# Performance work log

Hardware: AMD Instinct MI355X
Metric: run time of the kernel (lower is better)

## Reference

```python
import jax, jax.numpy as jnp
import numpy as np

N_SPARSE = 2  # keep N of every M weights (2:4 structured sparsity)
M_SPARSE = 4


def compute_mask(w, n, m):
    # w: [out, in]; zero the (m - n) smallest-|w| entries in each group of m
    out_f, in_f = w.shape
    k = m - n
    wr = jnp.abs(w).reshape(out_f, in_f // m, m)
    # indices of the k smallest |w| per group (torch.topk largest=False)
    _, idx = jax.lax.top_k(-wr, k)                      # [out, in/m, k]
    pruned = jax.nn.one_hot(idx, m, dtype=w.dtype).sum(axis=-2)  # [out, in/m, m]
    mask = 1.0 - pruned
    return mask.reshape(out_f, in_f)


def setup_inputs() -> dict:
    key = jax.random.key(0)
    k1, k2, k3 = jax.random.split(key, 3)
    B, S, Din, Dout = 64, 197, 768, 3072
    x = jax.random.normal(k1, (B, S, Din), dtype=jnp.float32)
    weight = jax.random.normal(k2, (Dout, Din), dtype=jnp.float32)
    bias = jax.random.normal(k3, (Dout,), dtype=jnp.float32)
    return {"x": x, "weight": weight, "bias": bias}


def reference(x, weight, bias):
    # mask is a precomputed buffer in torch (not differentiated)
    mask = compute_mask(jax.lax.stop_gradient(weight), N_SPARSE, M_SPARSE)
    w = weight * mask
    # F.linear: x @ w.T + b
    return jnp.einsum('bsi,oi->bso', x, w) + bias
```

## Files before the change

### kernel.cpp

```cpp
#include <hip/hip_runtime.h>
#include <hip/hip_bf16.h>

#define M_DIM 12608
#define K_DIM 768
#define N_DIM 3072
#define M_PAD 12800
#define BM 128
#define BN 128
#define BK 32
#define NT (K_DIM / BK)
#define MBLK (M_PAD / BM)
#define NBLK (N_DIM / BN)
#define NWG (MBLK * NBLK)

typedef __attribute__((ext_vector_type(8))) short bf16x8;
typedef __attribute__((ext_vector_type(4))) float f32x4;

__device__ __forceinline__ void gload_lds16(const void* g, void* l) {
  __builtin_amdgcn_global_load_lds(
      (const __attribute__((address_space(1))) unsigned int*)g,
      (__attribute__((address_space(3))) unsigned int*)l,
      16, 0, 0);
}

#define GX 4800
#define GW 2304
__global__ void cvt_fused(const float* __restrict__ x, const float* __restrict__ w,
                          __hip_bfloat16* __restrict__ xb, __hip_bfloat16* __restrict__ wb) {
  if (blockIdx.x < GX) {
    size_t i = ((size_t)blockIdx.x * 256 + threadIdx.x) * 8;
    union { __hip_bfloat16 h[8]; uint4 u; } o;
    if (i < (size_t)M_DIM * K_DIM) {
      float4 a = *(const float4*)(x + i);
      float4 b = *(const float4*)(x + i + 4);
      o.h[0] = __float2bfloat16(a.x); o.h[1] = __float2bfloat16(a.y);
      o.h[2] = __float2bfloat16(a.z); o.h[3] = __float2bfloat16(a.w);
      o.h[4] = __float2bfloat16(b.x); o.h[5] = __float2bfloat16(b.y);
      o.h[6] = __float2bfloat16(b.z); o.h[7] = __float2bfloat16(b.w);
    } else {
      o.u = make_uint4(0, 0, 0, 0);
    }
    *(uint4*)(xb + i) = o.u;
  } else {
    size_t g = ((size_t)(blockIdx.x - GX) * 256 + threadIdx.x);
    float4 v = *(const float4*)(w + g * 4);
    float val[4] = {v.x, v.y, v.z, v.w};
    float a[4] = {fabsf(v.x), fabsf(v.y), fabsf(v.z), fabsf(v.w)};
    union { __hip_bfloat16 h[4]; uint2 u; } o;
#pragma unroll
    for (int i = 0; i < 4; ++i) {
      int rank = 0;
#pragma unroll
      for (int j = 0; j < 4; ++j)
        rank += (a[j] > a[i]) || (a[j] == a[i] && j > i);
      o.h[i] = __float2bfloat16(rank < 2 ? val[i] : 0.0f);
    }
    *(uint2*)(wb + g * 4) = o.u;
  }
}

__global__ __launch_bounds__(256, 4) void gemm_bt(
    const __hip_bfloat16* __restrict__ A,
    const __hip_bfloat16* __restrict__ B,
    const float* __restrict__ bias,
    float* __restrict__ C)
{
  __shared__ char smem[32768];

  const int tid  = threadIdx.x;
  const int lane = tid & 63;
  const int wave = tid >> 6;
  const int wm   = wave >> 1;
  const int wn   = wave & 1;

  const int wg  = blockIdx.x;
  const int swz = (wg & 7) * (NWG / 8) + (wg >> 3);
  const int tile_m = (swz / NBLK) * BM;
  const int tile_n = (swz % NBLK) * BN;

  const int r2 = lane >> 2;
  const int p  = lane & 3;
  const int gsw = p ^ (r2 & 3) ^ ((r2 >> 2) & 3);
  const __hip_bfloat16* asrc[2];
  const __hip_bfloat16* bsrc[2];
#pragma unroll
  for (int u = 0; u < 2; ++u) {
    const int row = wave * 32 + u * 16 + r2;
    asrc[u] = A + (size_t)(tile_m + row) * K_DIM + gsw * 8;
    bsrc[u] = B + (size_t)(tile_n + row) * K_DIM + gsw * 8;
  }

  const int frow  = lane & 15;
  const int fslot = (lane >> 4) ^ (frow & 3) ^ ((frow >> 2) & 3);
  const int abase = (wm * 64 + frow) * 64 + fslot * 16;
  const int bbase = 8192 + (wn * 64 + frow) * 64 + fslot * 16;

  f32x4 acc[4][4] = {};

#pragma unroll
  for (int u = 0; u < 2; ++u)
    gload_lds16(asrc[u], smem + (wave * 2 + u) * 1024);
#pragma unroll
  for (int u = 0; u < 2; ++u)
    gload_lds16(bsrc[u], smem + 8192 + (wave * 2 + u) * 1024);

  for (int t = 0; t < NT; ++t) {
    __syncthreads();

    if (t + 1 < NT) {
      char* nb = smem + ((t + 1) & 1) * 16384;
      const int off = (t + 1) * BK;
#pragma unroll
      for (int u = 0; u < 2; ++u)
        gload_lds16(asrc[u] + off, nb + (wave * 2 + u) * 1024);
#pragma unroll
      for (int u = 0; u < 2; ++u)
        gload_lds16(bsrc[u] + off, nb + 8192 + (wave * 2 + u) * 1024);
    }

    const char* bq = smem + (t & 1) * 16384;
    bf16x8 af[4], bfv[4];
#pragma unroll
    for (int m = 0; m < 4; ++m)
      af[m] = *(const bf16x8*)(bq + abase + m * 1024);
#pragma unroll
    for (int n = 0; n < 4; ++n)
      bfv[n] = *(const bf16x8*)(bq + bbase + n * 1024);
#pragma unroll
    for (int m = 0; m < 4; ++m)
#pragma unroll
      for (int n = 0; n < 4; ++n)
        acc[m][n] = __builtin_amdgcn_mfma_f32_16x16x32_bf16(af[m], bfv[n], acc[m][n], 0, 0, 0);
  }

  const int ccol = lane & 15;
  const int quad = lane >> 4;
  float bv[4];
#pragma unroll
  for (int n = 0; n < 4; ++n)
    bv[n] = bias[tile_n + wn * 64 + n * 16 + ccol];

#pragma unroll
  for (int m = 0; m < 4; ++m) {
    const int rbase = tile_m + wm * 64 + m * 16 + quad * 4;
#pragma unroll
    for (int r = 0; r < 4; ++r) {
      const int grow = rbase + r;
      if (grow < M_DIM) {
        float* crow = C + (size_t)grow * N_DIM + tile_n + wn * 64;
#pragma unroll
        for (int n = 0; n < 4; ++n)
          crow[n * 16 + ccol] = acc[m][n][r] + bv[n];
      }
    }
  }
}

extern "C" void kernel_launch(void* const* d_in, const int* in_sizes, int n_in,
                              void* d_out, int out_size, void* d_ws, size_t ws_size,
                              hipStream_t stream) {
  const float* x    = (const float*)d_in[0];
  const float* w    = (const float*)d_in[1];
  const float* bias = (const float*)d_in[2];
  float* out = (float*)d_out;

  __hip_bfloat16* xb = (__hip_bfloat16*)d_ws;
  __hip_bfloat16* wb = xb + (size_t)M_PAD * K_DIM;

  cvt_fused<<<GX + GW, 256, 0, stream>>>(x, w, xb, wb);
  gemm_bt<<<NWG, 256, 0, stream>>>(xb, wb, bias, out);
}
```

Baseline: 249.0 us.

## Rewrite GEMM as 256x256 tile, 8-wave ping-pong pipeline with barriers and setprio

Replaces the 128x128 tile, 4-wave GEMM with a 256x256x64 tile run by 8 waves over 128KB of dynamic LDS. The loop interleaves staged global-to-LDS loads with MFMA quarters, using explicit vmcnt waits, barriers and s_setprio to overlap memory traffic with matrix math. The larger tiles raise arithmetic intensity and cut redundant global loads. The cost is more registers per thread (acc[8][4]), lower occupancy, fewer workgroups (50x12=600) which can hurt wave quantization, and fragile hand-written synchronisation.

```diff
diff --git a/kernel.cpp b/kernel.cpp
--- a/kernel.cpp
+++ b/kernel.cpp
@@ -5,9 +5,9 @@
 #define K_DIM 768
 #define N_DIM 3072
 #define M_PAD 12800
-#define BM 128
-#define BN 128
-#define BK 32
+#define BM 256
+#define BN 256
+#define BK 64
 #define NT (K_DIM / BK)
 #define MBLK (M_PAD / BM)
 #define NBLK (N_DIM / BN)
@@ -59,78 +59,117 @@
   }
 }
 
-__global__ __launch_bounds__(256, 4) void gemm_bt(
+__global__ __launch_bounds__(512, 2) void gemm_8p(
     const __hip_bfloat16* __restrict__ A,
     const __hip_bfloat16* __restrict__ B,
     const float* __restrict__ bias,
     float* __restrict__ C)
 {
-  __shared__ char smem[32768];
+  extern __shared__ char smem[];
 
   const int tid  = threadIdx.x;
   const int lane = tid & 63;
   const int wave = tid >> 6;
-  const int wm   = wave >> 1;
-  const int wn   = wave & 1;
+  const int wm   = wave >> 2;
+  const int wn   = wave & 3;
 
   const int wg  = blockIdx.x;
   const int swz = (wg & 7) * (NWG / 8) + (wg >> 3);
-  const int tile_m = (swz / NBLK) * BM;
-  const int tile_n = (swz % NBLK) * BN;
-
-  const int r2 = lane >> 2;
-  const int p  = lane & 3;
-  const int gsw = p ^ (r2 & 3) ^ ((r2 >> 2) & 3);
-  const __hip_bfloat16* asrc[2];
-  const __hip_bfloat16* bsrc[2];
-#pragma unroll
-  for (int u = 0; u < 2; ++u) {
-    const int row = wave * 32 + u * 16 + r2;
-    asrc[u] = A + (size_t)(tile_m + row) * K_DIM + gsw * 8;
-    bsrc[u] = B + (size_t)(tile_n + row) * K_DIM + gsw * 8;
-  }
-
-  const int frow  = lane & 15;
-  const int fslot = (lane >> 4) ^ (frow & 3) ^ ((frow >> 2) & 3);
-  const int abase = (wm * 64 + frow) * 64 + fslot * 16;
-  const int bbase = 8192 + (wn * 64 + frow) * 64 + fslot * 16;
-
-  f32x4 acc[4][4] = {};
-
-#pragma unroll
-  for (int u = 0; u < 2; ++u)
-    gload_lds16(asrc[u], smem + (wave * 2 + u) * 1024);
-#pragma unroll
-  for (int u = 0; u < 2; ++u)
-    gload_lds16(bsrc[u], smem + 8192 + (wave * 2 + u) * 1024);
-
-  for (int t = 0; t < NT; ++t) {
-    __syncthreads();
-
-    if (t + 1 < NT) {
-      char* nb = smem + ((t + 1) & 1) * 16384;
-      const int off = (t + 1) * BK;
-#pragma unroll
-      for (int u = 0; u < 2; ++u)
-        gload_lds16(asrc[u] + off, nb + (wave * 2 + u) * 1024);
-#pragma unroll
-      for (int u = 0; u < 2; ++u)
-        gload_lds16(bsrc[u] + off, nb + 8192 + (wave * 2 + u) * 1024);
-    }
-
-    const char* bq = smem + (t & 1) * 16384;
-    bf16x8 af[4], bfv[4];
-#pragma unroll
-    for (int m = 0; m < 4; ++m)
-      af[m] = *(const bf16x8*)(bq + abase + m * 1024);
-#pragma unroll
-    for (int n = 0; n < 4; ++n)
-      bfv[n] = *(const bf16x8*)(bq + bbase + n * 1024);
-#pragma unroll
-    for (int m = 0; m < 4; ++m)
-#pragma unroll
-      for (int n = 0; n < 4; ++n)
-        acc[m][n] = __builtin_amdgcn_mfma_f32_16x16x32_bf16(af[m], bfv[n], acc[m][n], 0, 0, 0);
+  const int tile_m = (swz % MBLK) * BM;
+  const int tile_n = (swz / MBLK) * BN;
+
+  const int l4 = lane >> 2;
+  const int gk = ((lane & 3) ^ ((lane >> 3) & 3)) * 8;
+  const __hip_bfloat16* ag = A + (size_t)(tile_m + wave * 16 + l4) * K_DIM + gk;
+  const __hip_bfloat16* bg = B + (size_t)(tile_n + wave * 16 + l4) * K_DIM + gk;
+
+#define STG_A(T, kh) { \
+    char* d_ = smem + (((T) & 1) << 16) + ((kh) << 14) + (wave << 10); \
+    gload_lds16(ag + (size_t)(T) * BK + (kh) * 32, d_); \
+    gload_lds16(ag + (size_t)128 * K_DIM + (size_t)(T) * BK + (kh) * 32, d_ + 8192); }
+#define STG_B(T, kh) { \
+    char* d_ = smem + (((T) & 1) << 16) + 32768 + ((kh) << 14) + (wave << 10); \
+    gload_lds16(bg + (size_t)(T) * BK + (kh) * 32, d_); \
+    gload_lds16(bg + (size_t)128 * K_DIM + (size_t)(T) * BK + (kh) * 32, d_ + 8192); }
+#define BAR() { __builtin_amdgcn_s_barrier(); asm volatile("" ::: "memory"); }
+#define VM(n) asm volatile("s_waitcnt vmcnt(" #n ")" ::: "memory")
+
+  const int frow = lane & 15;
+  const int fsl  = (((lane >> 4) ^ ((frow >> 1) & 3)) << 4);
+  const char* aL = smem + (wm * 128 + frow) * 64 + fsl;
+  const char* bL = smem + 32768 + (wn * 64 + frow) * 64 + fsl;
+
+  f32x4 acc[8][4] = {};
+  bf16x8 af[4], bfv[4];
+
+#define MFMA_Q(mbase) \
+    _Pragma("unroll") for (int m = 0; m < 4; ++m) \
+    _Pragma("unroll") for (int n = 0; n < 4; ++n) \
+      acc[(mbase) + m][n] = __builtin_amdgcn_mfma_f32_16x16x32_bf16(af[m], bfv[n], acc[(mbase) + m][n], 0, 0, 0);
+#define LD_A(db, kh, mbase) \
+    _Pragma("unroll") for (int m = 0; m < 4; ++m) \
+      af[m] = *(const bf16x8*)(aL + (db) + ((kh) << 14) + ((mbase) + m) * 1024);
+#define LD_B(db, kh) \
+    _Pragma("unroll") for (int n = 0; n < 4; ++n) \
+      bfv[n] = *(const bf16x8*)(bL + (db) + ((kh) << 14) + n * 1024);
+
+  STG_A(0, 0); STG_B(0, 0); STG_A(0, 1); STG_B(0, 1); STG_A(1, 0); STG_B(1, 0);
+  VM(8);
+  BAR();
+
+#pragma unroll 2
+  for (int t = 0; t < NT - 2; ++t) {
+    const int db = (t & 1) << 16;
+    LD_A(db, 0, 0); LD_B(db, 0);
+    STG_A(t + 1, 1);
+    BAR();
+    __builtin_amdgcn_s_setprio(1); MFMA_Q(0); __builtin_amdgcn_s_setprio(0);
+    BAR();
+    LD_A(db, 0, 4);
+    STG_B(t + 1, 1);
+    BAR();
+    __builtin_amdgcn_s_setprio(1); MFMA_Q(4); __builtin_amdgcn_s_setprio(0);
+    VM(8);
+    BAR();
+    LD_A(db, 1, 0); LD_B(db, 1);
+    STG_A(t + 2, 0);
+    BAR();
+    __builtin_amdgcn_s_setprio(1); MFMA_Q(0); __builtin_amdgcn_s_setprio(0);
+    BAR();
+    LD_A(db, 1, 4);
+    STG_B(t + 2, 0);
+    BAR();
+    __builtin_amdgcn_s_setprio(1); MFMA_Q(4); __builtin_amdgcn_s_setprio(0);
+    VM(8);
+    BAR();
+  }
+
+  {
+    const int db = ((NT - 2) & 1) << 16;
+    LD_A(db, 0, 0); LD_B(db, 0);
+    STG_A(NT - 1, 1);
+    BAR(); __builtin_amdgcn_s_setprio(1); MFMA_Q(0); __builtin_amdgcn_s_setprio(0); BAR();
+    LD_A(db, 0, 4);
+    STG_B(NT - 1, 1);
+    BAR(); __builtin_amdgcn_s_setprio(1); MFMA_Q(4); __builtin_amdgcn_s_setprio(0);
+    VM(8); BAR();
+    LD_A(db, 1, 0); LD_B(db, 1);
+    BAR(); __builtin_amdgcn_s_setprio(1); MFMA_Q(0); __builtin_amdgcn_s_setprio(0); BAR();
+    LD_A(db, 1, 4);
+    BAR(); __builtin_amdgcn_s_setprio(1); MFMA_Q(4); __builtin_amdgcn_s_setprio(0);
+    VM(4); BAR();
+  }
+  {
+    const int db = ((NT - 1) & 1) << 16;
+    LD_A(db, 0, 0); LD_B(db, 0);
+    BAR(); __builtin_amdgcn_s_setprio(1); MFMA_Q(0); __builtin_amdgcn_s_setprio(0); BAR();
+    LD_A(db, 0, 4);
+    BAR(); __builtin_amdgcn_s_setprio(1); MFMA_Q(4); __builtin_amdgcn_s_setprio(0);
+    VM(0); BAR();
+    LD_A(db, 1, 0); LD_B(db, 1);
+    BAR(); __builtin_amdgcn_s_setprio(1); MFMA_Q(0); __builtin_amdgcn_s_setprio(0); BAR();
+    LD_A(db, 1, 4);
+    __builtin_amdgcn_s_setprio(1); MFMA_Q(4); __builtin_amdgcn_s_setprio(0);
   }
 
   const int ccol = lane & 15;
@@ -141,8 +180,8 @@
     bv[n] = bias[tile_n + wn * 64 + n * 16 + ccol];
 
 #pragma unroll
-  for (int m = 0; m < 4; ++m) {
-    const int rbase = tile_m + wm * 64 + m * 16 + quad * 4;
+  for (int m = 0; m < 8; ++m) {
+    const int rbase = tile_m + wm * 128 + m * 16 + quad * 4;
 #pragma unroll
     for (int r = 0; r < 4; ++r) {
       const int grow = rbase + r;
@@ -167,6 +206,13 @@
   __hip_bfloat16* xb = (__hip_bfloat16*)d_ws;
   __hip_bfloat16* wb = xb + (size_t)M_PAD * K_DIM;
 
+  static bool attr_set = false;
+  if (!attr_set) {
+    hipFuncSetAttribute(reinterpret_cast<const void*>(gemm_8p),
+                        hipFuncAttributeMaxDynamicSharedMemorySize, 131072);
+    attr_set = true;
+  }
+
   cvt_fused<<<GX + GW, 256, 0, stream>>>(x, w, xb, wb);
-  gemm_bt<<<NWG, 256, 0, stream>>>(xb, wb, bias, out);
-}
+  gemm_8p<<<NWG, 512, 131072, stream>>>(xb, wb, bias, out);
+}
```

Result: no change. 250.5 us (+0.6%).
